# Kernel optimization log

Measured on AMD Instinct MI355X. Metric: run time of the kernel, lower is better.

The kernel has to match this reference:

```python
import jax, jax.numpy as jnp
import numpy as np

N = {"M": 100000, "E": 40000, "S": 20000}
IN_FEATS = 768
OUT_FEATS = 768
E_REL = 250000
RELS = ["M_M", "M_E", "M_S", "E_S", "E_M", "S_M", "S_E", "S_S", "E_E"]

def setup_inputs() -> dict:
    key = jax.random.key(0)
    ks = iter(jax.random.split(key, 64))
    inp = {}
    for t in ("M", "E", "S"):
        inp[f"x_{t}"] = jax.random.normal(next(ks), (N[t], IN_FEATS), jnp.float32)
    for r in RELS:
        s, d = r.split("_")
        inp[f"src_{r}"] = jax.random.randint(next(ks), (E_REL,), 0, N[s], jnp.int32)
        inp[f"dst_{r}"] = jax.random.randint(next(ks), (E_REL,), 0, N[d], jnp.int32)
        inp[f"w_{r}"] = jax.random.uniform(next(ks), (E_REL,), jnp.float32)
        inp[f"W_{r}"] = jax.random.normal(next(ks), (IN_FEATS, OUT_FEATS), jnp.float32) / np.float32(np.sqrt(IN_FEATS))
        inp[f"b_{r}"] = jnp.zeros((OUT_FEATS,), jnp.float32)
    return inp

def _graph_conv(x_src, src, dst, w, W, b, n_src, n_dst):
    # DGL GraphConv(norm='both') with per-edge weights: symmetric degree
    # normalization uses UNWEIGHTED relation-graph degrees, clamped >= 1.
    out_deg = jnp.maximum(jnp.zeros((n_src,), x_src.dtype).at[src].add(1.0), 1.0)
    in_deg = jnp.maximum(jnp.zeros((n_dst,), x_src.dtype).at[dst].add(1.0), 1.0)
    h = (x_src * (out_deg ** -0.5)[:, None]) @ W             # dense GEMM [n_src, out]
    msg = h[src] * w[:, None]                                 # gather + edge-weight mul
    agg = jax.ops.segment_sum(msg, dst, num_segments=n_dst)   # scatter-add SpMM
    return agg * (in_deg ** -0.5)[:, None] + b

def reference(x_M, x_E, x_S,
              src_M_M, dst_M_M, w_M_M, W_M_M, b_M_M,
              src_M_E, dst_M_E, w_M_E, W_M_E, b_M_E,
              src_M_S, dst_M_S, w_M_S, W_M_S, b_M_S,
              src_E_S, dst_E_S, w_E_S, W_E_S, b_E_S,
              src_E_M, dst_E_M, w_E_M, W_E_M, b_E_M,
              src_S_M, dst_S_M, w_S_M, W_S_M, b_S_M,
              src_S_E, dst_S_E, w_S_E, W_S_E, b_S_E,
              src_S_S, dst_S_S, w_S_S, W_S_S, b_S_S,
              src_E_E, dst_E_E, w_E_E, W_E_E, b_E_E):
    args = dict(locals())
    xs = {"M": x_M, "E": x_E, "S": x_S}
    acc = {t: jnp.zeros((N[t], OUT_FEATS), jnp.float32) for t in ("M", "E", "S")}
    for r in RELS:
        s, d = r.split("_")
        acc[d] = acc[d] + _graph_conv(xs[s], args[f"src_{r}"], args[f"dst_{r}"],
                                      args[f"w_{r}"], args[f"W_{r}"], args[f"b_{r}"],
                                      N[s], N[d])
    # HeteroGraphConv aggregate='sum', then per-type ReLU; outputs concatenated [M; E; S]
    return jnp.concatenate([jax.nn.relu(acc["M"]), jax.nn.relu(acc["E"]), jax.nn.relu(acc["S"])], axis=0)
```

## Files before the change

kernel.cpp:

```cpp
#include <hip/hip_runtime.h>
#include <stdint.h>

typedef short short8 __attribute__((ext_vector_type(8)));
typedef float floatx4 __attribute__((ext_vector_type(4)));

__device__ __forceinline__ float bf2f(unsigned short u) {
    union { unsigned int u; float f; } c; c.u = ((unsigned int)u) << 16; return c.f;
}
__device__ __forceinline__ unsigned short f2bf(float f) {
    union { float f; unsigned int u; } c; c.f = f;
    unsigned int u = c.u;
    unsigned int r = (u + 0x7fffu + ((u >> 16) & 1u)) >> 16;
    return (unsigned short)r;
}

__device__ __forceinline__ void gload16(const unsigned short* g, unsigned short* l) {
    __builtin_amdgcn_global_load_lds(
        (const __attribute__((address_space(1))) unsigned int*)g,
        (__attribute__((address_space(3))) unsigned int*)l,
        16, 0, 0);
}

__global__ __launch_bounds__(256) void k_zero(int* __restrict__ p, int n) {
    int i = blockIdx.x * 256 + threadIdx.x;
    int stride = gridDim.x * 256;
    for (; i < n; i += stride) p[i] = 0;
}

__global__ __launch_bounds__(256) void k_cvt_x(const float* __restrict__ x,
                                               unsigned short* __restrict__ xb,
                                               long long n4) {
    long long i = (long long)blockIdx.x * blockDim.x + threadIdx.x;
    long long stride = (long long)gridDim.x * blockDim.x;
    for (; i < n4; i += stride) {
        float4 v = ((const float4*)x)[i];
        ushort4 o;
        o.x = f2bf(v.x); o.y = f2bf(v.y); o.z = f2bf(v.z); o.w = f2bf(v.w);
        ((ushort4*)xb)[i] = o;
    }
}

__global__ __launch_bounds__(256) void k_twt(const float* __restrict__ W,
                                             unsigned short* __restrict__ Wt) {
    __shared__ float tile[32][33];
    int bn = blockIdx.x * 32;
    int bk = blockIdx.y * 32;
    int tx = threadIdx.x;
    int ty = threadIdx.y;
    for (int i = ty; i < 32; i += 8)
        tile[i][tx] = W[(size_t)(bk + i) * 768 + bn + tx];
    __syncthreads();
    for (int i = ty; i < 32; i += 8)
        Wt[(size_t)(bn + i) * 768 + bk + tx] = f2bf(tile[tx][i]);
}

__global__ __launch_bounds__(256) void k_deg(const int* __restrict__ s, const int* __restrict__ d,
                                             int* od, int* id, int ne) {
    int e = blockIdx.x * 256 + threadIdx.x;
    if (e < ne) { atomicAdd(&od[s[e]], 1); atomicAdd(&id[d[e]], 1); }
}

__global__ __launch_bounds__(256) void k_cnt(const int* __restrict__ id1, const int* __restrict__ id2,
                                             const int* __restrict__ id3,
                                             int* __restrict__ cnt, int* __restrict__ start,
                                             int* __restrict__ cur, int* cursor, int n) {
    int i = blockIdx.x * 256 + threadIdx.x;
    int c = 0;
    if (i < n) {
        c = id1[i] + id2[i] + id3[i];
        cnt[i] = c;
        cur[i] = 0;
    }
    int lane = threadIdx.x & 63;
    int v = c;
    #pragma unroll
    for (int off = 1; off < 64; off <<= 1) {
        int u = __shfl_up(v, off, 64);
        if (lane >= off) v += u;
    }
    int total = __shfl(v, 63, 64);
    int base = 0;
    if (lane == 63) base = atomicAdd(cursor, total);
    base = __shfl(base, 63, 64);
    if (i < n) start[i] = base + v - c;
}

__global__ __launch_bounds__(256) void k_fill(const int* __restrict__ src, const int* __restrict__ dst,
                                              const float* __restrict__ w,
                                              const int* __restrict__ od, const int* __restrict__ id,
                                              const int* __restrict__ start, int* cur,
                                              int2* __restrict__ e2, int soff, int ne) {
    int e = blockIdx.x * 256 + threadIdx.x;
    if (e >= ne) return;
    int s = src[e], d = dst[e];
    int pos = start[d] + atomicAdd(&cur[d], 1);
    int odv = od[s]; if (odv < 1) odv = 1;
    int idv = id[d]; if (idv < 1) idv = 1;
    float c = w[e] * rsqrtf((float)odv) * rsqrtf((float)idv);
    int2 rec; rec.x = soff + s; rec.y = __float_as_int(c);
    e2[pos] = rec;
}

__global__ __launch_bounds__(256) void k_gemm(const unsigned short* __restrict__ A,
                                              const unsigned short* __restrict__ Bt,
                                              unsigned short* __restrict__ C,
                                              int Mrows) {
    __shared__ __align__(16) unsigned short As[128 * 32];
    __shared__ __align__(16) unsigned short Bs[128 * 32];
    const int tid = threadIdx.x;
    const int m0 = blockIdx.x * 128;
    const int n0 = blockIdx.y * 128;
    const int lane = tid & 63;
    const int wave = tid >> 6;
    const int wm = (wave >> 1) * 64;
    const int wn = (wave & 1) * 64;
    const int l16 = lane & 15;
    const int quad = lane >> 4;

    floatx4 acc[4][4];
    #pragma unroll
    for (int i = 0; i < 4; i++)
        #pragma unroll
        for (int j = 0; j < 4; j++) acc[i][j] = (floatx4){0.f, 0.f, 0.f, 0.f};

    const int l0 = tid;
    const int l1 = tid + 256;
    const int r0 = l0 >> 2, c0 = (l0 & 3) * 8;
    const int r1 = l1 >> 2, c1 = (l1 & 3) * 8;
    int ar0 = m0 + r0; if (ar0 >= Mrows) ar0 = Mrows - 1;
    int ar1 = m0 + r1; if (ar1 >= Mrows) ar1 = Mrows - 1;
    const unsigned short* Ag0 = A + (size_t)ar0 * 768 + c0;
    const unsigned short* Ag1 = A + (size_t)ar1 * 768 + c1;
    const unsigned short* Bg0 = Bt + (size_t)(n0 + r0) * 768 + c0;
    const unsigned short* Bg1 = Bt + (size_t)(n0 + r1) * 768 + c1;
    unsigned short* Al0 = As + wave * 512;
    unsigned short* Al1 = As + wave * 512 + 2048;
    unsigned short* Bl0 = Bs + wave * 512;
    unsigned short* Bl1 = Bs + wave * 512 + 2048;

    for (int k0 = 0; k0 < 768; k0 += 32) {
        __syncthreads();
        gload16(Ag0 + k0, Al0);
        gload16(Ag1 + k0, Al1);
        gload16(Bg0 + k0, Bl0);
        gload16(Bg1 + k0, Bl1);
        asm volatile("s_waitcnt vmcnt(0)" ::: "memory");
        __syncthreads();

        short8 af[4], bfr[4];
        #pragma unroll
        for (int mt = 0; mt < 4; mt++)
            af[mt] = *(const short8*)&As[(wm + mt * 16 + l16) * 32 + quad * 8];
        #pragma unroll
        for (int nt = 0; nt < 4; nt++)
            bfr[nt] = *(const short8*)&Bs[(wn + nt * 16 + l16) * 32 + quad * 8];
        #pragma unroll
        for (int mt = 0; mt < 4; mt++)
            #pragma unroll
            for (int nt = 0; nt < 4; nt++)
                acc[mt][nt] = __builtin_amdgcn_mfma_f32_16x16x32_bf16(af[mt], bfr[nt], acc[mt][nt], 0, 0, 0);
    }

    #pragma unroll
    for (int mt = 0; mt < 4; mt++) {
        #pragma unroll
        for (int nt = 0; nt < 4; nt++) {
            const int gr0 = m0 + wm + mt * 16 + quad * 4;
            const int gc = n0 + wn + nt * 16 + l16;
            #pragma unroll
            for (int r = 0; r < 4; r++) {
                int gr = gr0 + r;
                if (gr < Mrows)
                    C[(size_t)gr * 768 + gc] = f2bf(acc[mt][nt][r]);
            }
        }
    }
}

__global__ __launch_bounds__(192) void k_agg(const unsigned short* __restrict__ Z,
                                             const int* __restrict__ start, const int* __restrict__ cnt,
                                             const int2* __restrict__ e2,
                                             const float* __restrict__ b1, const float* __restrict__ b2,
                                             const float* __restrict__ b3,
                                             float* __restrict__ out, int n) {
    int node = blockIdx.x;
    if (node >= n) return;
    int t = threadIdx.x;
    int c0 = t * 4;
    int s = start[node];
    int e = s + cnt[node];
    float ax = 0.f, ay = 0.f, az = 0.f, aw = 0.f;
    for (int i = s; i < e; i++) {
        int2 ed = e2[i];
        float c = __int_as_float(ed.y);
        ushort4 v = *(const ushort4*)(Z + (size_t)ed.x * 768 + c0);
        ax += c * bf2f(v.x);
        ay += c * bf2f(v.y);
        az += c * bf2f(v.z);
        aw += c * bf2f(v.w);
    }
    float4 o;
    o.x = ax + b1[c0 + 0] + b2[c0 + 0] + b3[c0 + 0];
    o.y = ay + b1[c0 + 1] + b2[c0 + 1] + b3[c0 + 1];
    o.z = az + b1[c0 + 2] + b2[c0 + 2] + b3[c0 + 2];
    o.w = aw + b1[c0 + 3] + b2[c0 + 3] + b3[c0 + 3];
    o.x = fmaxf(o.x, 0.f); o.y = fmaxf(o.y, 0.f);
    o.z = fmaxf(o.z, 0.f); o.w = fmaxf(o.w, 0.f);
    *(float4*)(out + (size_t)node * 768 + c0) = o;
}

extern "C" void kernel_launch(void* const* d_in, const int* in_sizes, int n_in,
                              void* d_out, int out_size, void* d_ws, size_t ws_size,
                              hipStream_t stream) {
    const int NM = 100000, NE = 40000, NS = 20000;
    const int EREL = 250000;
    (void)in_sizes; (void)n_in; (void)out_size;

    const float* xM = (const float*)d_in[0];
    const float* xE = (const float*)d_in[1];
    const float* xS = (const float*)d_in[2];
    const int* src[9]; const int* dst[9];
    const float* w[9]; const float* W[9]; const float* b[9];
    for (int r = 0; r < 9; r++) {
        src[r] = (const int*)d_in[3 + 5 * r + 0];
        dst[r] = (const int*)d_in[3 + 5 * r + 1];
        w[r]   = (const float*)d_in[3 + 5 * r + 2];
        W[r]   = (const float*)d_in[3 + 5 * r + 3];
        b[r]   = (const float*)d_in[3 + 5 * r + 4];
    }

    const size_t XB_OFF = 0;
    const size_t Z_OFF  = 245760000;
    const size_t WT_OFF = 491520000;
    const size_t OD_OFF = 502136832;
    const size_t ID_OFF = 505736832;
    const size_t CURSOR_OFF = 509336832;
    const size_t CNT_OFF = 509337088;
    const size_t START_OFF = 509737088;
    const size_t CUR_OFF = 510137088;
    const size_t E2_OFF = 510537088;
    const size_t WS_NEEDED = 516537088;
    if (ws_size < WS_NEEDED) return;

    char* ws = (char*)d_ws;
    unsigned short* Xb = (unsigned short*)(ws + XB_OFF);
    unsigned short* Z  = (unsigned short*)(ws + Z_OFF);
    unsigned short* Wt = (unsigned short*)(ws + WT_OFF);
    int* od     = (int*)(ws + OD_OFF);
    int* id     = (int*)(ws + ID_OFF);
    int* cursor = (int*)(ws + CURSOR_OFF);
    int* cnt    = (int*)(ws + CNT_OFF);
    int* start  = (int*)(ws + START_OFF);
    int* cur    = (int*)(ws + CUR_OFF);
    int2* e2    = (int2*)(ws + E2_OFF);

    const int rel_soff[9] = {0, 0, 0, 100000, 100000, 140000, 140000, 140000, 100000};
    const int rel_nsrc[9] = {NM, NM, NM, NE, NE, NS, NS, NS, NE};
    const int phase_nd[3]  = {NM, NE, NS};
    const int phase_out[3] = {0, 100000, 140000};
    const int phase_rels[3][3] = { {0, 4, 5}, {1, 8, 6}, {2, 3, 7} };

    k_zero<<<1760, 256, 0, stream>>>(od, 1800064);

    const int eblk = (EREL + 255) / 256;
    for (int r = 0; r < 9; r++)
        k_deg<<<eblk, 256, 0, stream>>>(src[r], dst[r], od + r * 100000, id + r * 100000, EREL);

    k_cvt_x<<<4096, 256, 0, stream>>>(xM, Xb, (long long)NM * 768 / 4);
    k_cvt_x<<<2048, 256, 0, stream>>>(xE, Xb + (size_t)100000 * 768, (long long)NE * 768 / 4);
    k_cvt_x<<<1024, 256, 0, stream>>>(xS, Xb + (size_t)140000 * 768, (long long)NS * 768 / 4);

    for (int r = 0; r < 9; r++)
        k_twt<<<dim3(24, 24), dim3(32, 8), 0, stream>>>(W[r], Wt + (size_t)r * 589824);

    for (int p = 0; p < 3; p++) {
        const int nd = phase_nd[p];
        const int r0 = phase_rels[p][0], r1 = phase_rels[p][1], r2 = phase_rels[p][2];

        for (int j = 0; j < 3; j++) {
            int r = phase_rels[p][j];
            dim3 g((rel_nsrc[r] + 127) / 128, 6);
            k_gemm<<<g, 256, 0, stream>>>(Xb + (size_t)rel_soff[r] * 768,
                                          Wt + (size_t)r * 589824,
                                          Z + (size_t)rel_soff[r] * 768,
                                          rel_nsrc[r]);
        }

        k_cnt<<<(nd + 255) / 256, 256, 0, stream>>>(id + r0 * 100000, id + r1 * 100000,
                                                    id + r2 * 100000, cnt, start, cur, cursor + p, nd);
        for (int j = 0; j < 3; j++) {
            int r = phase_rels[p][j];
            k_fill<<<eblk, 256, 0, stream>>>(src[r], dst[r], w[r],
                                             od + r * 100000, id + r * 100000,
                                             start, cur, e2, rel_soff[r], EREL);
        }
        k_agg<<<nd, 192, 0, stream>>>(Z, start, cnt, e2, b[r0], b[r1], b[r2],
                                      (float*)d_out + (size_t)phase_out[p] * 768, nd);
    }
}
```

Measured before the change: 2.892 ms.

## Batch per-relation kernels into single launches and fuse per-phase GEMMs

Merges the nine degree, three conversion, nine weight-transpose and three fill launches into one launch each, passing per-relation pointers through argument structs indexed by grid dimension. The three per-phase GEMMs become one launch over all 160000 source rows, which relies on Wt slots reordered so each phase's three weights are contiguous. A swizzled block index spreads tiles across XCDs. This cuts launch count and tail idle time between small kernels, at the cost of hardcoded sizes and extra per-block index arithmetic.

```diff
diff --git a/kernel.cpp b/kernel.cpp
--- a/kernel.cpp
+++ b/kernel.cpp
@@ -21,28 +21,42 @@
         16, 0, 0);
 }
 
+struct DegArgs { const int* s[9]; const int* d[9]; };
+struct TwtArgs { const float* W[9]; int slot[9]; };
+struct CvtArgs { const float* xM; const float* xE; const float* xS; };
+struct FillArgs {
+    const int* src[3]; const int* dst[3]; const float* w[3];
+    const int* od[3]; const int* id[3]; int soff[3];
+};
+
 __global__ __launch_bounds__(256) void k_zero(int* __restrict__ p, int n) {
     int i = blockIdx.x * 256 + threadIdx.x;
     int stride = gridDim.x * 256;
     for (; i < n; i += stride) p[i] = 0;
 }
 
-__global__ __launch_bounds__(256) void k_cvt_x(const float* __restrict__ x,
-                                               unsigned short* __restrict__ xb,
-                                               long long n4) {
+__global__ __launch_bounds__(256) void k_cvt_all(CvtArgs P, unsigned short* __restrict__ xb) {
+    const long long NM4 = 19200000LL;
+    const long long NE4 = 26880000LL;
+    const long long NT4 = 30720000LL;
     long long i = (long long)blockIdx.x * blockDim.x + threadIdx.x;
     long long stride = (long long)gridDim.x * blockDim.x;
-    for (; i < n4; i += stride) {
-        float4 v = ((const float4*)x)[i];
+    for (; i < NT4; i += stride) {
+        float4 v;
+        if (i < NM4)       v = ((const float4*)P.xM)[i];
+        else if (i < NE4)  v = ((const float4*)P.xE)[i - NM4];
+        else               v = ((const float4*)P.xS)[i - NE4];
         ushort4 o;
         o.x = f2bf(v.x); o.y = f2bf(v.y); o.z = f2bf(v.z); o.w = f2bf(v.w);
         ((ushort4*)xb)[i] = o;
     }
 }
 
-__global__ __launch_bounds__(256) void k_twt(const float* __restrict__ W,
-                                             unsigned short* __restrict__ Wt) {
+__global__ __launch_bounds__(256) void k_twt_all(TwtArgs P, unsigned short* __restrict__ WtBase) {
     __shared__ float tile[32][33];
+    int r = blockIdx.z;
+    const float* W = P.W[r];
+    unsigned short* Wt = WtBase + (size_t)P.slot[r] * 589824;
     int bn = blockIdx.x * 32;
     int bk = blockIdx.y * 32;
     int tx = threadIdx.x;
@@ -54,10 +68,13 @@
         Wt[(size_t)(bn + i) * 768 + bk + tx] = f2bf(tile[tx][i]);
 }
 
-__global__ __launch_bounds__(256) void k_deg(const int* __restrict__ s, const int* __restrict__ d,
-                                             int* od, int* id, int ne) {
+__global__ __launch_bounds__(256) void k_deg_all(DegArgs P, int* __restrict__ od, int* __restrict__ id, int ne) {
+    int r = blockIdx.y;
     int e = blockIdx.x * 256 + threadIdx.x;
-    if (e < ne) { atomicAdd(&od[s[e]], 1); atomicAdd(&id[d[e]], 1); }
+    if (e < ne) {
+        atomicAdd(&od[r * 100000 + P.s[r][e]], 1);
+        atomicAdd(&id[r * 100000 + P.d[r][e]], 1);
+    }
 }
 
 __global__ __launch_bounds__(256) void k_cnt(const int* __restrict__ id1, const int* __restrict__ id2,
@@ -85,31 +102,37 @@
     if (i < n) start[i] = base + v - c;
 }
 
-__global__ __launch_bounds__(256) void k_fill(const int* __restrict__ src, const int* __restrict__ dst,
-                                              const float* __restrict__ w,
-                                              const int* __restrict__ od, const int* __restrict__ id,
-                                              const int* __restrict__ start, int* cur,
-                                              int2* __restrict__ e2, int soff, int ne) {
+__global__ __launch_bounds__(256) void k_fill3(FillArgs P,
+                                               const int* __restrict__ start, int* cur,
+                                               int2* __restrict__ e2, int ne) {
+    int j = blockIdx.y;
     int e = blockIdx.x * 256 + threadIdx.x;
     if (e >= ne) return;
-    int s = src[e], d = dst[e];
+    int s = P.src[j][e], d = P.dst[j][e];
     int pos = start[d] + atomicAdd(&cur[d], 1);
-    int odv = od[s]; if (odv < 1) odv = 1;
-    int idv = id[d]; if (idv < 1) idv = 1;
-    float c = w[e] * rsqrtf((float)odv) * rsqrtf((float)idv);
-    int2 rec; rec.x = soff + s; rec.y = __float_as_int(c);
+    int odv = P.od[j][s]; if (odv < 1) odv = 1;
+    int idv = P.id[j][d]; if (idv < 1) idv = 1;
+    float c = P.w[j][e] * rsqrtf((float)odv) * rsqrtf((float)idv);
+    int2 rec; rec.x = P.soff[j] + s; rec.y = __float_as_int(c);
     e2[pos] = rec;
 }
 
-__global__ __launch_bounds__(256) void k_gemm(const unsigned short* __restrict__ A,
-                                              const unsigned short* __restrict__ Bt,
-                                              unsigned short* __restrict__ C,
-                                              int Mrows) {
+__global__ __launch_bounds__(256) void k_gemmf(const unsigned short* __restrict__ A,
+                                               const unsigned short* __restrict__ WtP,
+                                               unsigned short* __restrict__ Z) {
     __shared__ __align__(16) unsigned short As[128 * 32];
     __shared__ __align__(16) unsigned short Bs[128 * 32];
+    const int bid = blockIdx.x;
+    const int s = (bid & 7) * 939 + (bid >> 3);
+    const int mb = s / 6;
+    const int n0 = (s - mb * 6) * 128;
+    int row0, rend, slot;
+    if (mb < 782)        { row0 = mb * 128;                  rend = 100000; slot = 0; }
+    else if (mb < 1095)  { row0 = 100000 + (mb - 782) * 128; rend = 140000; slot = 1; }
+    else                 { row0 = 140000 + (mb - 1095) * 128; rend = 160000; slot = 2; }
+    const unsigned short* Bt = WtP + (size_t)slot * 589824;
+
     const int tid = threadIdx.x;
-    const int m0 = blockIdx.x * 128;
-    const int n0 = blockIdx.y * 128;
     const int lane = tid & 63;
     const int wave = tid >> 6;
     const int wm = (wave >> 1) * 64;
@@ -127,8 +150,8 @@
     const int l1 = tid + 256;
     const int r0 = l0 >> 2, c0 = (l0 & 3) * 8;
     const int r1 = l1 >> 2, c1 = (l1 & 3) * 8;
-    int ar0 = m0 + r0; if (ar0 >= Mrows) ar0 = Mrows - 1;
-    int ar1 = m0 + r1; if (ar1 >= Mrows) ar1 = Mrows - 1;
+    int ar0 = row0 + r0; if (ar0 >= rend) ar0 = rend - 1;
+    int ar1 = row0 + r1; if (ar1 >= rend) ar1 = rend - 1;
     const unsigned short* Ag0 = A + (size_t)ar0 * 768 + c0;
     const unsigned short* Ag1 = A + (size_t)ar1 * 768 + c1;
     const unsigned short* Bg0 = Bt + (size_t)(n0 + r0) * 768 + c0;
@@ -165,13 +188,13 @@
     for (int mt = 0; mt < 4; mt++) {
         #pragma unroll
         for (int nt = 0; nt < 4; nt++) {
-            const int gr0 = m0 + wm + mt * 16 + quad * 4;
+            const int gr0 = row0 + wm + mt * 16 + quad * 4;
             const int gc = n0 + wn + nt * 16 + l16;
             #pragma unroll
             for (int r = 0; r < 4; r++) {
                 int gr = gr0 + r;
-                if (gr < Mrows)
-                    C[(size_t)gr * 768 + gc] = f2bf(acc[mt][nt][r]);
+                if (gr < rend)
+                    Z[(size_t)gr * 768 + gc] = f2bf(acc[mt][nt][r]);
             }
         }
     }
@@ -255,7 +278,7 @@
     int2* e2    = (int2*)(ws + E2_OFF);
 
     const int rel_soff[9] = {0, 0, 0, 100000, 100000, 140000, 140000, 140000, 100000};
-    const int rel_nsrc[9] = {NM, NM, NM, NE, NE, NS, NS, NS, NE};
+    const int wtslot[9] = {0, 3, 6, 7, 1, 2, 5, 8, 4};
     const int phase_nd[3]  = {NM, NE, NS};
     const int phase_out[3] = {0, 100000, 140000};
     const int phase_rels[3][3] = { {0, 4, 5}, {1, 8, 6}, {2, 3, 7} };
@@ -263,37 +286,34 @@
     k_zero<<<1760, 256, 0, stream>>>(od, 1800064);
 
     const int eblk = (EREL + 255) / 256;
-    for (int r = 0; r < 9; r++)
-        k_deg<<<eblk, 256, 0, stream>>>(src[r], dst[r], od + r * 100000, id + r * 100000, EREL);
-
-    k_cvt_x<<<4096, 256, 0, stream>>>(xM, Xb, (long long)NM * 768 / 4);
-    k_cvt_x<<<2048, 256, 0, stream>>>(xE, Xb + (size_t)100000 * 768, (long long)NE * 768 / 4);
-    k_cvt_x<<<1024, 256, 0, stream>>>(xS, Xb + (size_t)140000 * 768, (long long)NS * 768 / 4);
-
-    for (int r = 0; r < 9; r++)
-        k_twt<<<dim3(24, 24), dim3(32, 8), 0, stream>>>(W[r], Wt + (size_t)r * 589824);
+    DegArgs dp;
+    for (int r = 0; r < 9; r++) { dp.s[r] = src[r]; dp.d[r] = dst[r]; }
+    k_deg_all<<<dim3(eblk, 9), 256, 0, stream>>>(dp, od, id, EREL);
+
+    CvtArgs cp; cp.xM = xM; cp.xE = xE; cp.xS = xS;
+    k_cvt_all<<<4096, 256, 0, stream>>>(cp, Xb);
+
+    TwtArgs tp;
+    for (int r = 0; r < 9; r++) { tp.W[r] = W[r]; tp.slot[r] = wtslot[r]; }
+    k_twt_all<<<dim3(24, 24, 9), dim3(32, 8), 0, stream>>>(tp, Wt);
 
     for (int p = 0; p < 3; p++) {
         const int nd = phase_nd[p];
         const int r0 = phase_rels[p][0], r1 = phase_rels[p][1], r2 = phase_rels[p][2];
 
+        k_gemmf<<<7512, 256, 0, stream>>>(Xb, Wt + (size_t)p * 3 * 589824, Z);
+
+        k_cnt<<<(nd + 255) / 256, 256, 0, stream>>>(id + r0 * 100000, id + r1 * 100000,
+                                                    id + r2 * 100000, cnt, start, cur, cursor + p, nd);
+        FillArgs fp;
         for (int j = 0; j < 3; j++) {
             int r = phase_rels[p][j];
-            dim3 g((rel_nsrc[r] + 127) / 128, 6);
-            k_gemm<<<g, 256, 0, stream>>>(Xb + (size_t)rel_soff[r] * 768,
-                                          Wt + (size_t)r * 589824,
-                                          Z + (size_t)rel_soff[r] * 768,
-                                          rel_nsrc[r]);
+            fp.src[j] = src[r]; fp.dst[j] = dst[r]; fp.w[j] = w[r];
+            fp.od[j] = od + r * 100000; fp.id[j] = id + r * 100000;
+            fp.soff[j] = rel_soff[r];
         }
-
-        k_cnt<<<(nd + 255) / 256, 256, 0, stream>>>(id + r0 * 100000, id + r1 * 100000,
-                                                    id + r2 * 100000, cnt, start, cur, cursor + p, nd);
-        for (int j = 0; j < 3; j++) {
-            int r = phase_rels[p][j];
-            k_fill<<<eblk, 256, 0, stream>>>(src[r], dst[r], w[r],
-                                             od + r * 100000, id + r * 100000,
-                                             start, cur, e2, rel_soff[r], EREL);
-        }
+        k_fill3<<<dim3(eblk, 3), 256, 0, stream>>>(fp, start, cur, e2, EREL);
+
         k_agg<<<nd, 192, 0, stream>>>(Z, start, cnt, e2, b[r0], b[r1], b[r2],
                                       (float*)d_out + (size_t)phase_out[p] * 768, nd);
     }
```

New measurement: 2.643 ms. 8.6% less time.
